# Kernel optimization log

Hardware: AMD Instinct MI355X
Metric: run time of the kernel (lower is better)

Reference implementation:

```python
import jax, jax.numpy as jnp
import numpy as np

IN_DIM = 256   # opt.word_vec_size
MEM_DIM = 256  # opt.rnn_size // num_directions
N_LEAVES = 131072  # 2**17, complete binary tree


def setup_inputs() -> dict:
    key = jax.random.key(0)
    ks = jax.random.split(key, 8)
    s = 0.05  # weight scale
    return {
        # leaf word2vec embeddings, in-order leaf sequence of the tree
        "x": jax.random.normal(ks[0], (N_LEAVES, IN_DIM), jnp.float32),
        # BinaryTreeLeafModule params (Linear as x @ W + b)
        "Wcx": jax.random.normal(ks[1], (IN_DIM, MEM_DIM), jnp.float32) * s,
        "bcx": jnp.zeros((MEM_DIM,), jnp.float32),
        "Wox": jax.random.normal(ks[2], (IN_DIM, MEM_DIM), jnp.float32) * s,
        "box": jnp.zeros((MEM_DIM,), jnp.float32),
        # BinaryTreeComposer params: 4 left-child gates (i, lf, rf, u) fused
        # along the output dim, likewise 4 right-child gates.
        "Wl": jax.random.normal(ks[3], (MEM_DIM, 4 * MEM_DIM), jnp.float32) * s,
        "bl": jnp.zeros((4 * MEM_DIM,), jnp.float32),
        "Wr": jax.random.normal(ks[4], (MEM_DIM, 4 * MEM_DIM), jnp.float32) * s,
        "br": jnp.zeros((4 * MEM_DIM,), jnp.float32),
        "lengths": N_LEAVES,  # max sequence length for output padding
    }


def reference(x, Wcx, bcx, Wox, box, Wl, bl, Wr, br, lengths):
    m = Wcx.shape[1]
    # ---- BinaryTreeLeafModule, batched over all leaves ----
    c = x @ Wcx + bcx                                   # [n, m]
    h = jax.nn.sigmoid(x @ Wox + box) * jnp.tanh(c)     # [n, m]
    leaf_h = h  # in-order cat of leaf outputs == recursive cat([lo, ro])

    # ---- BinaryTreeComposer, one batched step per tree level ----
    # Loop over log2(n_leaves) levels of a complete binary tree; each
    # iteration composes adjacent sibling pairs (shapes static -> jit-safe).
    while c.shape[0] > 1:
        lc, rc = c[0::2], c[1::2]
        lh, rh = h[0::2], h[1::2]
        g = (lh @ Wl + bl) + (rh @ Wr + br)             # [n/2, 4m]
        gi, glf, grf, gu = jnp.split(g, 4, axis=-1)
        i = jax.nn.sigmoid(gi)
        lf = jax.nn.sigmoid(glf)
        rf = jax.nn.sigmoid(grf)
        u = jnp.tanh(gu)
        c = i * u + lf * lc + rf * rc                   # [n/2, m]
        h = jnp.tanh(c)                                 # gate_output=False

    # ---- root post-processing (as in original when tree.parent is None) ----
    output = leaf_h[:, None, :]                         # [n_leaves, 1, m]
    supl = int(lengths) - output.shape[0]
    if supl > 0:
        output = jnp.concatenate(
            [output, jnp.zeros((supl, 1, m), output.dtype)], axis=0)
    c_root = c[:, None, :]                              # [1, 1, m]
    h_root = h[:, None, :]                              # [1, 1, m]
    return output, (c_root, h_root)
```

## Files before the change

### kernel.cpp

```cpp
#include <hip/hip_runtime.h>
#include <cstdint>
#include <cstddef>


typedef float floatx4 __attribute__((ext_vector_type(4)));
typedef __bf16 bf16x8 __attribute__((ext_vector_type(8)));

typedef __attribute__((address_space(1))) unsigned int u32g;
typedef __attribute__((address_space(3))) unsigned int u32l;

__device__ __forceinline__ void async_copy16(const void* g, void* l) {
  __builtin_amdgcn_global_load_lds((u32g*)(uintptr_t)g, (u32l*)l, 16, 0, 0);
}

__device__ __forceinline__ float sigf(float x) {
  return __builtin_amdgcn_rcpf(1.f + __expf(-x));
}
__device__ __forceinline__ float tanh_f(float x) {
  float e = __expf(-2.f * x);
  return __builtin_fmaf(2.f, __builtin_amdgcn_rcpf(1.f + e), -1.f);
}

__global__ void prep_leaf(const float* __restrict__ Wcx, const float* __restrict__ bcx,
                          const float* __restrict__ Wox, const float* __restrict__ box,
                          __bf16* __restrict__ WleafT, float* __restrict__ bleaf) {
  int n = blockIdx.x;
  int k = threadIdx.x;
  const float* src = (n < 256) ? Wcx : Wox;
  int col = n & 255;
  WleafT[n * 256 + k] = (__bf16)src[k * 256 + col];
  if (k == 0) bleaf[n] = (n < 256) ? bcx[col] : box[col];
}

__global__ void prep_cat(const float* __restrict__ Wl, const float* __restrict__ bl,
                         const float* __restrict__ Wr, const float* __restrict__ br,
                         __bf16* __restrict__ WcatT, float* __restrict__ bcat) {
  int n = blockIdx.x;
  for (int k = threadIdx.x; k < 512; k += 256) {
    const float* src = (k < 256) ? Wl : Wr;
    WcatT[n * 512 + k] = (__bf16)src[(size_t)(k & 255) * 1024 + n];
  }
  if (threadIdx.x == 0) bcat[n] = bl[n] + br[n];
}

__global__ __launch_bounds__(256, 2) void leaf_kernel(
    const float* __restrict__ x,
    const __bf16* __restrict__ WT,
    const float* __restrict__ bleaf,
    __bf16* __restrict__ c_out,
    __bf16* __restrict__ h_out,
    float* __restrict__ h_out32)
{
  __shared__ __bf16 SMEM[32768];
  const int tid  = threadIdx.x;
  const int wave = tid >> 6;
  const int lane = tid & 63;
  const int quad = lane >> 4;
  const int l15  = lane & 15;

  const int lid = blockIdx.y * gridDim.x + blockIdx.x;
  const int nwg = gridDim.x * gridDim.y;
  const int swz = (lid & 7) * (nwg >> 3) + (lid >> 3);
  const int j0  = (swz & 3) * 64;
  const int bm  = swz >> 2;

  floatx4 acc[2][8];
#pragma unroll
  for (int r = 0; r < 2; ++r)
#pragma unroll
    for (int f = 0; f < 8; ++f) acc[r][f] = (floatx4){0.f, 0.f, 0.f, 0.f};

  float4 pa[4][2];

#pragma unroll
  for (int it = 0; it < 4; ++it) {
    int f = it * 256 + tid;
    int row = f >> 3, cc = f & 7;
    int cb = cc ^ (row & 7);
    const float4* gx = (const float4*)(x + (size_t)(bm * 128 + row) * 256 + cc * 8);
    pa[it][0] = gx[0]; pa[it][1] = gx[1];
    int ng = ((row >> 6) << 8) + j0 + (row & 63);
    async_copy16(WT + (size_t)ng * 256 + cb * 8, &SMEM[8192 + (f & ~63) * 8]);
  }
#pragma unroll
  for (int it = 0; it < 4; ++it) {
    int f = it * 256 + tid;
    int row = f >> 3, cc = f & 7;
    int cb = cc ^ (row & 7);
    float4 u = pa[it][0], v = pa[it][1];
    bf16x8 a8 = {(__bf16)u.x, (__bf16)u.y, (__bf16)u.z, (__bf16)u.w,
                 (__bf16)v.x, (__bf16)v.y, (__bf16)v.z, (__bf16)v.w};
    *(bf16x8*)&SMEM[row * 64 + cb * 8] = a8;
  }
  __syncthreads();

#pragma unroll
  for (int t = 0; t < 4; ++t) {
    const int cur = (t & 1) * 16384;
    const int nxt = 16384 - cur;
    if (t < 3) {
      const int kk = (t + 1) * 64;
#pragma unroll
      for (int it = 0; it < 4; ++it) {
        int f = it * 256 + tid;
        int row = f >> 3, cc = f & 7;
        int cb = cc ^ (row & 7);
        const float4* gx = (const float4*)(x + (size_t)(bm * 128 + row) * 256 + kk + cc * 8);
        pa[it][0] = gx[0]; pa[it][1] = gx[1];
        int ng = ((row >> 6) << 8) + j0 + (row & 63);
        async_copy16(WT + (size_t)ng * 256 + kk + cb * 8, &SMEM[nxt + 8192 + (f & ~63) * 8]);
      }
    }
#pragma unroll
    for (int s = 0; s < 2; ++s) {
      const int b  = (s * 4 + quad) ^ (l15 & 7);
      const int kb = b * 8;
      bf16x8 a0 = *(const bf16x8*)&SMEM[cur + (wave * 32 + l15) * 64 + kb];
      bf16x8 a1 = *(const bf16x8*)&SMEM[cur + (wave * 32 + 16 + l15) * 64 + kb];
#pragma unroll
      for (int f = 0; f < 8; ++f) {
        bf16x8 b8 = *(const bf16x8*)&SMEM[cur + 8192 + (f * 16 + l15) * 64 + kb];
        acc[0][f] = __builtin_amdgcn_mfma_f32_16x16x32_bf16(a0, b8, acc[0][f], 0, 0, 0);
        acc[1][f] = __builtin_amdgcn_mfma_f32_16x16x32_bf16(a1, b8, acc[1][f], 0, 0, 0);
      }
    }
    if (t < 3) {
#pragma unroll
      for (int it = 0; it < 4; ++it) {
        int f = it * 256 + tid;
        int row = f >> 3, cc = f & 7;
        int cb = cc ^ (row & 7);
        float4 u = pa[it][0], v = pa[it][1];
        bf16x8 a8 = {(__bf16)u.x, (__bf16)u.y, (__bf16)u.z, (__bf16)u.w,
                     (__bf16)v.x, (__bf16)v.y, (__bf16)v.z, (__bf16)v.w};
        *(bf16x8*)&SMEM[nxt + row * 64 + cb * 8] = a8;
      }
    }
    __syncthreads();
  }

  const int R0 = bm * 128;
#pragma unroll
  for (int r = 0; r < 2; ++r) {
#pragma unroll
    for (int q = 0; q < 4; ++q) {
      int col = j0 + q * 16 + l15;
      float bC = bleaf[col];
      float bO = bleaf[256 + col];
#pragma unroll
      for (int reg = 0; reg < 4; ++reg) {
        int lr = wave * 32 + r * 16 + quad * 4 + reg;
        int lc = q * 16 + l15;
        float c = acc[r][q][reg] + bC;
        float o = acc[r][q + 4][reg] + bO;
        float h = sigf(o) * tanh_f(c);
        h_out32[(size_t)(R0 + lr) * 256 + col] = h;
        int ch  = (lc >> 3) ^ ((lr ^ (lr >> 3)) & 7);
        int idx = lr * 64 + ch * 8 + (lc & 7);
        SMEM[idx]        = (__bf16)c;
        SMEM[8192 + idx] = (__bf16)h;
      }
    }
  }
  __syncthreads();
#pragma unroll
  for (int i = 0; i < 4; ++i) {
    int unit = i * 256 + tid;
    int lr = unit >> 3, k = unit & 7;
    int ch = k ^ ((lr ^ (lr >> 3)) & 7);
    bf16x8 vc = *(const bf16x8*)&SMEM[lr * 64 + ch * 8];
    bf16x8 vh = *(const bf16x8*)&SMEM[8192 + lr * 64 + ch * 8];
    size_t g = (size_t)(R0 + lr) * 256 + j0 + k * 8;
    *(bf16x8*)&c_out[g] = vc;
    *(bf16x8*)&h_out[g] = vh;
  }
}

template <typename OUT>
__global__ __launch_bounds__(256, 2) void tree_level(
    const __bf16* __restrict__ h_in,
    const __bf16* __restrict__ c_in,
    const __bf16* __restrict__ WT,
    const float* __restrict__ bcat,
    OUT* __restrict__ c_out,
    OUT* __restrict__ h_out,
    const int M)
{
  __shared__ __bf16 SMEM[32768];
  const int tid  = threadIdx.x;
  const int wave = tid >> 6;
  const int lane = tid & 63;
  const int quad = lane >> 4;
  const int l15  = lane & 15;

  const int lid = blockIdx.y * gridDim.x + blockIdx.x;
  const int nwg = gridDim.x * gridDim.y;
  const int swz = (lid & 7) * (nwg >> 3) + (lid >> 3);
  const int j0  = (swz & 7) * 32;
  const int bm  = swz >> 3;

  floatx4 acc[2][8];
#pragma unroll
  for (int r = 0; r < 2; ++r)
#pragma unroll
    for (int f = 0; f < 8; ++f) acc[r][f] = (floatx4){0.f, 0.f, 0.f, 0.f};

#pragma unroll
  for (int it = 0; it < 4; ++it) {
    int f = it * 256 + tid;
    int row = f >> 3, cc = f & 7;
    int cb = cc ^ (row & 7);
    int rg = bm * 128 + row;
    rg = rg < M ? rg : M - 1;
    async_copy16(h_in + (size_t)rg * 512 + cb * 8, &SMEM[(f & ~63) * 8]);
    int ng = ((row >> 5) << 8) + j0 + (row & 31);
    async_copy16(WT + (size_t)ng * 512 + cb * 8, &SMEM[8192 + (f & ~63) * 8]);
  }
  __syncthreads();

#pragma unroll
  for (int t = 0; t < 8; ++t) {
    const int cur = (t & 1) * 16384;
    const int nxt = 16384 - cur;
    if (t < 7) {
      const int kk = (t + 1) * 64;
#pragma unroll
      for (int it = 0; it < 4; ++it) {
        int f = it * 256 + tid;
        int row = f >> 3, cc = f & 7;
        int cb = cc ^ (row & 7);
        int rg = bm * 128 + row;
        rg = rg < M ? rg : M - 1;
        async_copy16(h_in + (size_t)rg * 512 + kk + cb * 8, &SMEM[nxt + (f & ~63) * 8]);
        int ng = ((row >> 5) << 8) + j0 + (row & 31);
        async_copy16(WT + (size_t)ng * 512 + kk + cb * 8, &SMEM[nxt + 8192 + (f & ~63) * 8]);
      }
    }
#pragma unroll
    for (int s = 0; s < 2; ++s) {
      const int b  = (s * 4 + quad) ^ (l15 & 7);
      const int kb = b * 8;
      bf16x8 a0 = *(const bf16x8*)&SMEM[cur + (wave * 32 + l15) * 64 + kb];
      bf16x8 a1 = *(const bf16x8*)&SMEM[cur + (wave * 32 + 16 + l15) * 64 + kb];
#pragma unroll
      for (int f = 0; f < 8; ++f) {
        bf16x8 b8 = *(const bf16x8*)&SMEM[cur + 8192 + (f * 16 + l15) * 64 + kb];
        acc[0][f] = __builtin_amdgcn_mfma_f32_16x16x32_bf16(a0, b8, acc[0][f], 0, 0, 0);
        acc[1][f] = __builtin_amdgcn_mfma_f32_16x16x32_bf16(a1, b8, acc[1][f], 0, 0, 0);
      }
    }
    __syncthreads();
  }

  {
    const int maxr = 2 * M - 1;
#pragma unroll
    for (int i = 0; i < 4; ++i) {
      int chunk = i * 256 + tid;
      int row = chunk >> 2, piece = chunk & 3;
      int gr = bm * 256 + row;
      gr = gr < maxr ? gr : maxr;
      async_copy16(c_in + (size_t)gr * 256 + j0 + piece * 8,
                   &SMEM[16384 + (chunk & ~63) * 8]);
    }
  }
  __syncthreads();

  if constexpr (sizeof(OUT) == 2) {
#pragma unroll
    for (int r = 0; r < 2; ++r) {
#pragma unroll
      for (int q = 0; q < 2; ++q) {
        int col = j0 + q * 16 + l15;
        float bi  = bcat[col];
        float blf = bcat[256 + col];
        float brf = bcat[512 + col];
        float bu  = bcat[768 + col];
#pragma unroll
        for (int reg = 0; reg < 4; ++reg) {
          int lr  = wave * 32 + r * 16 + quad * 4 + reg;
          int lcc = q * 16 + l15;
          int row = bm * 128 + lr;
          float cn = 0.f, hn = 0.f;
          if (row < M) {
            float lc = (float)SMEM[16384 + (2 * lr) * 32 + lcc];
            float rc = (float)SMEM[16384 + (2 * lr + 1) * 32 + lcc];
            float iv = sigf(acc[r][0 + q][reg] + bi);
            float lf = sigf(acc[r][2 + q][reg] + blf);
            float rf = sigf(acc[r][4 + q][reg] + brf);
            float uv = tanh_f(acc[r][6 + q][reg] + bu);
            cn = iv * uv + lf * lc + rf * rc;
            hn = tanh_f(cn);
          }
          int ch  = (lcc >> 3) ^ ((lr ^ (lr >> 2)) & 3);
          int idx = lr * 32 + ch * 8 + (lcc & 7);
          SMEM[idx]        = (__bf16)cn;
          SMEM[4096 + idx] = (__bf16)hn;
        }
      }
    }
    __syncthreads();
#pragma unroll
    for (int i = 0; i < 2; ++i) {
      int unit = i * 256 + tid;
      int lr = unit >> 2, k = unit & 3;
      int gr = bm * 128 + lr;
      if (gr < M) {
        int ch = k ^ ((lr ^ (lr >> 2)) & 3);
        bf16x8 vc = *(const bf16x8*)&SMEM[lr * 32 + ch * 8];
        bf16x8 vh = *(const bf16x8*)&SMEM[4096 + lr * 32 + ch * 8];
        size_t g = (size_t)gr * 256 + j0 + k * 8;
        *(bf16x8*)((__bf16*)c_out + g) = vc;
        *(bf16x8*)((__bf16*)h_out + g) = vh;
      }
    }
  } else {
#pragma unroll
    for (int r = 0; r < 2; ++r) {
#pragma unroll
      for (int q = 0; q < 2; ++q) {
        int col = j0 + q * 16 + l15;
        float bi  = bcat[col];
        float blf = bcat[256 + col];
        float brf = bcat[512 + col];
        float bu  = bcat[768 + col];
#pragma unroll
        for (int reg = 0; reg < 4; ++reg) {
          int lr  = wave * 32 + r * 16 + quad * 4 + reg;
          int lcc = q * 16 + l15;
          int row = bm * 128 + lr;
          if (row < M) {
            float lc = (float)SMEM[16384 + (2 * lr) * 32 + lcc];
            float rc = (float)SMEM[16384 + (2 * lr + 1) * 32 + lcc];
            float iv = sigf(acc[r][0 + q][reg] + bi);
            float lf = sigf(acc[r][2 + q][reg] + blf);
            float rf = sigf(acc[r][4 + q][reg] + brf);
            float uv = tanh_f(acc[r][6 + q][reg] + bu);
            float cn = iv * uv + lf * lc + rf * rc;
            float hn = tanh_f(cn);
            size_t idx = (size_t)row * 256 + col;
            c_out[idx] = (OUT)cn;
            h_out[idx] = (OUT)hn;
          }
        }
      }
    }
  }
}

extern "C" void kernel_launch(void* const* d_in, const int* in_sizes, int n_in,
                              void* d_out, int out_size, void* d_ws, size_t ws_size,
                              hipStream_t stream) {
  const float* x   = (const float*)d_in[0];
  const float* Wcx = (const float*)d_in[1];
  const float* bcx = (const float*)d_in[2];
  const float* Wox = (const float*)d_in[3];
  const float* box = (const float*)d_in[4];
  const float* Wl  = (const float*)d_in[5];
  const float* bl  = (const float*)d_in[6];
  const float* Wr  = (const float*)d_in[7];
  const float* br  = (const float*)d_in[8];

  const size_t LEAF = (size_t)131072 * 256;
  const size_t MiB  = 1ull << 20;
  char* ws = (char*)d_ws;

  __bf16* WleafT = (__bf16*)(ws);
  __bf16* WcatT  = (__bf16*)(ws + 262144);
  float*  bleaf  = (float*)(ws + 262144 + 1048576);
  float*  bcat   = bleaf + 512;

  int slog = 17;
  size_t ra_sz = 0, rb_sz = 0;
  while (slog > 11) {
    size_t SL  = (size_t)1 << slog;
    size_t nsl = (size_t)(131072 >> slog);
    ra_sz = SL * 512 > nsl * 524288 ? SL * 512 : nsl * 524288;
    rb_sz = SL * 256 > nsl * 262144 ? SL * 256 : nsl * 262144;
    size_t need = 2 * MiB + SL * 1024 + ra_sz + rb_sz + nsl * MiB;
    if (need <= ws_size) break;
    --slog;
  }
  const int SLAB  = 1 << slog;
  const int nslab = 131072 >> slog;

  char*   dyn = ws + 2 * MiB;
  __bf16* LC  = (__bf16*)dyn;
  __bf16* LH  = LC + (size_t)SLAB * 256;
  char*   RA  = (char*)(LH + (size_t)SLAB * 256);
  char*   RB  = RA + ra_sz;
  __bf16* CC  = (__bf16*)(RB + rb_sz);
  __bf16* CH  = CC + (size_t)nslab * 1024 * 256;

  float* out    = (float*)d_out;
  float* leaf_h = out;
  float* c_root = out + LEAF;
  float* h_root = out + LEAF + 256;

  prep_leaf<<<dim3(512), dim3(256), 0, stream>>>(Wcx, bcx, Wox, box, WleafT, bleaf);
  prep_cat<<<dim3(1024), dim3(256), 0, stream>>>(Wl, bl, Wr, br, WcatT, bcat);

  if (nslab == 1) {
    leaf_kernel<<<dim3(4, SLAB / 128), dim3(256), 0, stream>>>(
        x, WleafT, bleaf, LC, LH, leaf_h);

    const __bf16* hin = LH;
    const __bf16* cin = LC;
    for (int lvl = 1; lvl <= slog; ++lvl) {
      const int M = SLAB >> lvl;
      dim3 grid(8, (M + 127) / 128);
      if (lvl == slog) {
        tree_level<float><<<grid, dim3(256), 0, stream>>>(
            hin, cin, WcatT, bcat, c_root, h_root, M);
      } else {
        __bf16* cdst = (__bf16*)((lvl & 1) ? RA : RB);
        __bf16* hdst = cdst + (size_t)M * 256;
        tree_level<__bf16><<<grid, dim3(256), 0, stream>>>(
            hin, cin, WcatT, bcat, cdst, hdst, M);
        hin = hdst; cin = cdst;
      }
    }
  } else {
    const int STOP = slog - 10;
    for (int sl = 0; sl < nslab; ++sl) {
      const size_t R0 = (size_t)sl * SLAB;
      leaf_kernel<<<dim3(4, SLAB / 128), dim3(256), 0, stream>>>(
          x + R0 * 256, WleafT, bleaf, LC, LH, leaf_h + R0 * 256);

      const __bf16* hin = LH;
      const __bf16* cin = LC;
      for (int lvl = 1; lvl <= STOP; ++lvl) {
        const int M = SLAB >> lvl;
        dim3 grid(8, (M + 127) / 128);
        __bf16 *cdst, *hdst;
        if (lvl == STOP) {
          cdst = CC + (size_t)sl * 1024 * 256;
          hdst = CH + (size_t)sl * 1024 * 256;
        } else {
          cdst = (__bf16*)((lvl & 1) ? RA : RB);
          hdst = cdst + (size_t)M * 256;
        }
        tree_level<__bf16><<<grid, dim3(256), 0, stream>>>(
            hin, cin, WcatT, bcat, cdst, hdst, M);
        hin = hdst; cin = cdst;
      }
    }
    {
      const __bf16* hin = CH;
      const __bf16* cin = CC;
      int pp = 1;
      for (int M = (nslab << 10) >> 1; M >= 1; M >>= 1, pp ^= 1) {
        dim3 grid(8, (M + 127) / 128);
        if (M == 1) {
          tree_level<float><<<grid, dim3(256), 0, stream>>>(
              hin, cin, WcatT, bcat, c_root, h_root, 1);
        } else {
          __bf16* cdst = (__bf16*)(pp ? RA : RB);
          __bf16* hdst = cdst + (size_t)M * 256;
          tree_level<__bf16><<<grid, dim3(256), 0, stream>>>(
              hin, cin, WcatT, bcat, cdst, hdst, M);
          hin = hdst; cin = cdst;
        }
      }
    }
  }
}
```

Baseline: 643.8 us.

## Single-buffer A tile through registers to cut LDS and fit three blocks per CU

Shared memory per block in the leaf and tree-level GEMM kernels drops from 64KB to 48KB. Only the weight tile stays double-buffered; the activation tile is staged in registers and written into one LDS buffer after an extra barrier. Launch bounds rise to three blocks per CU to raise occupancy. The tree kernel also issues the c_in child-cell load during the last K iteration so it overlaps the MFMA work. The costs are an additional __syncthreads per K step, less overlap of A-tile loads, and more register pressure that could cause spills.

```diff
diff --git a/kernel.cpp b/kernel.cpp
--- a/kernel.cpp
+++ b/kernel.cpp
@@ -43,7 +43,7 @@
   if (threadIdx.x == 0) bcat[n] = bl[n] + br[n];
 }
 
-__global__ __launch_bounds__(256, 2) void leaf_kernel(
+__global__ __launch_bounds__(256, 3) void leaf_kernel(
     const float* __restrict__ x,
     const __bf16* __restrict__ WT,
     const float* __restrict__ bleaf,
@@ -51,7 +51,7 @@
     __bf16* __restrict__ h_out,
     float* __restrict__ h_out32)
 {
-  __shared__ __bf16 SMEM[32768];
+  __shared__ __bf16 SMEM[24576];
   const int tid  = threadIdx.x;
   const int wave = tid >> 6;
   const int lane = tid & 63;
@@ -96,8 +96,8 @@
 
 #pragma unroll
   for (int t = 0; t < 4; ++t) {
-    const int cur = (t & 1) * 16384;
-    const int nxt = 16384 - cur;
+    const int curB = 8192 + (t & 1) * 8192;
+    const int nxtB = 8192 + ((t + 1) & 1) * 8192;
     if (t < 3) {
       const int kk = (t + 1) * 64;
 #pragma unroll
@@ -108,22 +108,23 @@
         const float4* gx = (const float4*)(x + (size_t)(bm * 128 + row) * 256 + kk + cc * 8);
         pa[it][0] = gx[0]; pa[it][1] = gx[1];
         int ng = ((row >> 6) << 8) + j0 + (row & 63);
-        async_copy16(WT + (size_t)ng * 256 + kk + cb * 8, &SMEM[nxt + 8192 + (f & ~63) * 8]);
+        async_copy16(WT + (size_t)ng * 256 + kk + cb * 8, &SMEM[nxtB + (f & ~63) * 8]);
       }
     }
 #pragma unroll
     for (int s = 0; s < 2; ++s) {
       const int b  = (s * 4 + quad) ^ (l15 & 7);
       const int kb = b * 8;
-      bf16x8 a0 = *(const bf16x8*)&SMEM[cur + (wave * 32 + l15) * 64 + kb];
-      bf16x8 a1 = *(const bf16x8*)&SMEM[cur + (wave * 32 + 16 + l15) * 64 + kb];
+      bf16x8 a0 = *(const bf16x8*)&SMEM[(wave * 32 + l15) * 64 + kb];
+      bf16x8 a1 = *(const bf16x8*)&SMEM[(wave * 32 + 16 + l15) * 64 + kb];
 #pragma unroll
       for (int f = 0; f < 8; ++f) {
-        bf16x8 b8 = *(const bf16x8*)&SMEM[cur + 8192 + (f * 16 + l15) * 64 + kb];
+        bf16x8 b8 = *(const bf16x8*)&SMEM[curB + (f * 16 + l15) * 64 + kb];
         acc[0][f] = __builtin_amdgcn_mfma_f32_16x16x32_bf16(a0, b8, acc[0][f], 0, 0, 0);
         acc[1][f] = __builtin_amdgcn_mfma_f32_16x16x32_bf16(a1, b8, acc[1][f], 0, 0, 0);
       }
     }
+    __syncthreads();
     if (t < 3) {
 #pragma unroll
       for (int it = 0; it < 4; ++it) {
@@ -133,10 +134,10 @@
         float4 u = pa[it][0], v = pa[it][1];
         bf16x8 a8 = {(__bf16)u.x, (__bf16)u.y, (__bf16)u.z, (__bf16)u.w,
                      (__bf16)v.x, (__bf16)v.y, (__bf16)v.z, (__bf16)v.w};
-        *(bf16x8*)&SMEM[nxt + row * 64 + cb * 8] = a8;
-      }
-    }
-    __syncthreads();
+        *(bf16x8*)&SMEM[row * 64 + cb * 8] = a8;
+      }
+      __syncthreads();
+    }
   }
 
   const int R0 = bm * 128;
@@ -177,7 +178,7 @@
 }
 
 template <typename OUT>
-__global__ __launch_bounds__(256, 2) void tree_level(
+__global__ __launch_bounds__(256, 3) void tree_level(
     const __bf16* __restrict__ h_in,
     const __bf16* __restrict__ c_in,
     const __bf16* __restrict__ WT,
@@ -186,7 +187,7 @@
     OUT* __restrict__ h_out,
     const int M)
 {
-  __shared__ __bf16 SMEM[32768];
+  __shared__ __bf16 SMEM[24576];
   const int tid  = threadIdx.x;
   const int wave = tid >> 6;
   const int lane = tid & 63;
@@ -204,6 +205,8 @@
   for (int r = 0; r < 2; ++r)
 #pragma unroll
     for (int f = 0; f < 8; ++f) acc[r][f] = (floatx4){0.f, 0.f, 0.f, 0.f};
+
+  bf16x8 pa[4];
 
 #pragma unroll
   for (int it = 0; it < 4; ++it) {
@@ -212,16 +215,22 @@
     int cb = cc ^ (row & 7);
     int rg = bm * 128 + row;
     rg = rg < M ? rg : M - 1;
-    async_copy16(h_in + (size_t)rg * 512 + cb * 8, &SMEM[(f & ~63) * 8]);
+    pa[it] = *(const bf16x8*)&h_in[(size_t)rg * 512 + cb * 8];
     int ng = ((row >> 5) << 8) + j0 + (row & 31);
     async_copy16(WT + (size_t)ng * 512 + cb * 8, &SMEM[8192 + (f & ~63) * 8]);
   }
+#pragma unroll
+  for (int it = 0; it < 4; ++it) {
+    int f = it * 256 + tid;
+    int row = f >> 3, cc = f & 7;
+    *(bf16x8*)&SMEM[row * 64 + cc * 8] = pa[it];
+  }
   __syncthreads();
 
 #pragma unroll
   for (int t = 0; t < 8; ++t) {
-    const int cur = (t & 1) * 16384;
-    const int nxt = 16384 - cur;
+    const int curB = 8192 + (t & 1) * 8192;
+    const int nxtB = 8192 + ((t + 1) & 1) * 8192;
     if (t < 7) {
       const int kk = (t + 1) * 64;
 #pragma unroll
@@ -231,40 +240,46 @@
         int cb = cc ^ (row & 7);
         int rg = bm * 128 + row;
         rg = rg < M ? rg : M - 1;
-        async_copy16(h_in + (size_t)rg * 512 + kk + cb * 8, &SMEM[nxt + (f & ~63) * 8]);
+        pa[it] = *(const bf16x8*)&h_in[(size_t)rg * 512 + kk + cb * 8];
         int ng = ((row >> 5) << 8) + j0 + (row & 31);
-        async_copy16(WT + (size_t)ng * 512 + kk + cb * 8, &SMEM[nxt + 8192 + (f & ~63) * 8]);
+        async_copy16(WT + (size_t)ng * 512 + kk + cb * 8, &SMEM[nxtB + (f & ~63) * 8]);
+      }
+    } else {
+      const int maxr = 2 * M - 1;
+#pragma unroll
+      for (int i = 0; i < 4; ++i) {
+        int chunk = i * 256 + tid;
+        int row = chunk >> 2, piece = chunk & 3;
+        int gr = bm * 256 + row;
+        gr = gr < maxr ? gr : maxr;
+        async_copy16(c_in + (size_t)gr * 256 + j0 + piece * 8,
+                     &SMEM[8192 + (chunk & ~63) * 8]);
       }
     }
 #pragma unroll
     for (int s = 0; s < 2; ++s) {
       const int b  = (s * 4 + quad) ^ (l15 & 7);
       const int kb = b * 8;
-      bf16x8 a0 = *(const bf16x8*)&SMEM[cur + (wave * 32 + l15) * 64 + kb];
-      bf16x8 a1 = *(const bf16x8*)&SMEM[cur + (wave * 32 + 16 + l15) * 64 + kb];
+      bf16x8 a0 = *(const bf16x8*)&SMEM[(wave * 32 + l15) * 64 + kb];
+      bf16x8 a1 = *(const bf16x8*)&SMEM[(wave * 32 + 16 + l15) * 64 + kb];
 #pragma unroll
       for (int f = 0; f < 8; ++f) {
-        bf16x8 b8 = *(const bf16x8*)&SMEM[cur + 8192 + (f * 16 + l15) * 64 + kb];
+        bf16x8 b8 = *(const bf16x8*)&SMEM[curB + (f * 16 + l15) * 64 + kb];
         acc[0][f] = __builtin_amdgcn_mfma_f32_16x16x32_bf16(a0, b8, acc[0][f], 0, 0, 0);
         acc[1][f] = __builtin_amdgcn_mfma_f32_16x16x32_bf16(a1, b8, acc[1][f], 0, 0, 0);
       }
     }
     __syncthreads();
-  }
-
-  {
-    const int maxr = 2 * M - 1;
-#pragma unroll
-    for (int i = 0; i < 4; ++i) {
-      int chunk = i * 256 + tid;
-      int row = chunk >> 2, piece = chunk & 3;
-      int gr = bm * 256 + row;
-      gr = gr < maxr ? gr : maxr;
-      async_copy16(c_in + (size_t)gr * 256 + j0 + piece * 8,
-                   &SMEM[16384 + (chunk & ~63) * 8]);
-    }
-  }
-  __syncthreads();
+    if (t < 7) {
+#pragma unroll
+      for (int it = 0; it < 4; ++it) {
+        int f = it * 256 + tid;
+        int row = f >> 3, cc = f & 7;
+        *(bf16x8*)&SMEM[row * 64 + cc * 8] = pa[it];
+      }
+      __syncthreads();
+    }
+  }
 
   if constexpr (sizeof(OUT) == 2) {
 #pragma unroll
@@ -283,8 +298,8 @@
           int row = bm * 128 + lr;
           float cn = 0.f, hn = 0.f;
           if (row < M) {
-            float lc = (float)SMEM[16384 + (2 * lr) * 32 + lcc];
-            float rc = (float)SMEM[16384 + (2 * lr + 1) * 32 + lcc];
+            float lc = (float)SMEM[8192 + (2 * lr) * 32 + lcc];
+            float rc = (float)SMEM[8192 + (2 * lr + 1) * 32 + lcc];
             float iv = sigf(acc[r][0 + q][reg] + bi);
             float lf = sigf(acc[r][2 + q][reg] + blf);
             float rf = sigf(acc[r][4 + q][reg] + brf);
@@ -330,8 +345,8 @@
           int lcc = q * 16 + l15;
           int row = bm * 128 + lr;
           if (row < M) {
-            float lc = (float)SMEM[16384 + (2 * lr) * 32 + lcc];
-            float rc = (float)SMEM[16384 + (2 * lr + 1) * 32 + lcc];
+            float lc = (float)SMEM[8192 + (2 * lr) * 32 + lcc];
+            float rc = (float)SMEM[8192 + (2 * lr + 1) * 32 + lcc];
             float iv = sigf(acc[r][0 + q][reg] + bi);
             float lf = sigf(acc[r][2 + q][reg] + blf);
             float rf = sigf(acc[r][4 + q][reg] + brf);
```

Result: slower. 661.0 us (+2.7%).
